# Performance work log

Hardware: AMD Instinct MI355X
Metric: run time of the kernel (lower is better)

## Reference

```python
import jax, jax.numpy as jnp
import numpy as np

N = 100000
E = 3200000
IN_C = 256
HID = 64
OUT_C = 2
EPS = 1e-5


def setup_inputs() -> dict:
    key = jax.random.key(0)
    ks = jax.random.split(key, 8)
    x = jax.random.normal(ks[0], (N, IN_C), dtype=jnp.float32)
    edge_index = jax.random.randint(ks[1], (2, E), 0, N, dtype=jnp.int64)
    # GCNConv weights (PyG: out = A_hat @ (x W) + b)
    W1 = jax.random.normal(ks[2], (IN_C, HID), dtype=jnp.float32) / np.sqrt(IN_C)
    b1 = jnp.zeros((HID,), dtype=jnp.float32)
    W2 = jax.random.normal(ks[3], (HID, OUT_C), dtype=jnp.float32) / np.sqrt(HID)
    b2 = jnp.zeros((OUT_C,), dtype=jnp.float32)
    # BatchNorm affine params
    g1 = jnp.ones((HID,), dtype=jnp.float32)
    be1 = jnp.zeros((HID,), dtype=jnp.float32)
    g2 = jnp.ones((OUT_C,), dtype=jnp.float32)
    be2 = jnp.zeros((OUT_C,), dtype=jnp.float32)
    # Decoder linear
    Wd = jax.random.normal(ks[4], (OUT_C, IN_C), dtype=jnp.float32) / np.sqrt(OUT_C)
    bd = jnp.zeros((IN_C,), dtype=jnp.float32)
    return {"x": x, "edge_index": edge_index, "W1": W1, "b1": b1, "g1": g1,
            "be1": be1, "W2": W2, "b2": b2, "g2": g2, "be2": be2,
            "Wd": Wd, "bd": bd}


def gcn_conv(x, W, b, src, dst, n):
    # x: [N, Cin] -> [N, Cout]; symmetric-normalized aggregation with self-loops
    xw = x @ W  # [N, Cout]
    loops = jnp.arange(n, dtype=src.dtype)
    s = jnp.concatenate([src, loops])  # [E+N]
    d = jnp.concatenate([dst, loops])
    deg = jax.ops.segment_sum(jnp.ones_like(d, dtype=x.dtype), d, num_segments=n)
    dinv = jax.lax.rsqrt(deg)  # deg >= 1 thanks to self-loops
    norm = dinv[s] * dinv[d]   # [E+N]
    out = jax.ops.segment_sum(norm[:, None] * xw[s], d, num_segments=n)
    return out + b


def batch_norm(x, gamma, beta):
    # training-mode BN over node dim, biased variance (torch semantics)
    mu = jnp.mean(x, axis=0)
    var = jnp.mean(jnp.square(x - mu), axis=0)
    return (x - mu) * jax.lax.rsqrt(var + EPS) * gamma + beta


def reference(x, edge_index, W1, b1, g1, be1, W2, b2, g2, be2, Wd, bd):
    src, dst = edge_index[0], edge_index[1]
    n = x.shape[0]
    h = gcn_conv(x, W1, b1, src, dst, n)
    h = jax.nn.relu(batch_norm(h, g1, be1))
    # dropout: identity (inference)
    z = batch_norm(gcn_conv(h, W2, b2, src, dst, n), g2, be2)
    return z @ Wd + bd  # decoder: [N, IN_C]
```

## Files before the change

kernel.cpp:

```cpp
#include <hip/hip_runtime.h>
#include <hip/hip_bf16.h>

#define NN 100000
#define NE 3200000
#define INC 256
#define HID 64
#define OUTC 2
#define EPSV 1e-5f

#define SCAN_CHUNK 1024
#define NBLK ((NN + SCAN_CHUNK - 1) / SCAN_CHUNK)

#define NBUCK 128
#define BCAP  26000
#define BIN_CHUNK 4096
#define BIN_K 16
#define BIN_GRID ((NE + BIN_CHUNK - 1) / BIN_CHUNK)

#define NQUART 25000

typedef short short8 __attribute__((ext_vector_type(8)));
typedef float f32x4 __attribute__((ext_vector_type(4)));

static __device__ __forceinline__ float bf2f(unsigned short u) {
    return __uint_as_float((unsigned)u << 16);
}
static __device__ __forceinline__ unsigned short f2bf(float f) {
    __hip_bfloat16 hb = __float2bfloat16(f);
    return *(unsigned short*)&hb;
}

__global__ __launch_bounds__(256) void bin_kernel(const int* __restrict__ src,
                                                  const int* __restrict__ dst,
                                                  int* __restrict__ gtail,
                                                  unsigned int* __restrict__ pbuf) {
    __shared__ int bcnt[NBUCK], bbase[NBUCK];
    int t = threadIdx.x;
    if (t < NBUCK) bcnt[t] = 0;
    __syncthreads();
    int base = blockIdx.x * BIN_CHUNK;
    int s[BIN_K], d[BIN_K], sl[BIN_K], bk[BIN_K];
#pragma unroll
    for (int r = 0; r < BIN_K; r++) {
        int i = base + r * 256 + t;
        bool v = i < NE;
        s[r] = v ? src[i] : 0;
        d[r] = v ? dst[i] : 0;
        bk[r] = (int)(((unsigned)d[r] * (unsigned)NBUCK) / (unsigned)NN);
        sl[r] = v ? atomicAdd(&bcnt[bk[r]], 1) : 0;
    }
    __syncthreads();
    if (t < NBUCK) bbase[t] = bcnt[t] ? atomicAdd(&gtail[t], bcnt[t]) : 0;
    __syncthreads();
#pragma unroll
    for (int r = 0; r < BIN_K; r++) {
        int i = base + r * 256 + t;
        if (i < NE) {
            int b = bk[r];
            int nbase = (b * NN + NBUCK - 1) >> 7;
            pbuf[(size_t)b * BCAP + bbase[b] + sl[r]] =
                ((unsigned)(d[r] - nbase) << 17) | (unsigned)s[r];
        }
    }
}

__global__ __launch_bounds__(256) void hist2_kernel(const unsigned int* __restrict__ pbuf,
                                                    const int* __restrict__ gtail,
                                                    int* __restrict__ cnt) {
    __shared__ int h[800];
    int b = blockIdx.x, t = threadIdx.x;
    int nb = (b * NN + NBUCK - 1) >> 7;
    int ne_ = ((b + 1) * NN + NBUCK - 1) >> 7;
    int range = ne_ - nb;
    for (int i = t; i < range; i += 256) h[i] = 0;
    __syncthreads();
    int ecnt = gtail[b];
    const unsigned int* p = pbuf + (size_t)b * BCAP;
    for (int i = t; i < ecnt; i += 256) atomicAdd(&h[p[i] >> 17], 1);
    __syncthreads();
    for (int i = t; i < range; i += 256) cnt[nb + i] = h[i];
}

__global__ void scan_btot_kernel(const int* __restrict__ cnt, int* __restrict__ btot) {
    __shared__ int red[4];
    int b = blockIdx.x, t = threadIdx.x;
    int base = b * SCAN_CHUNK;
    int v = 0;
    for (int j = t; j < SCAN_CHUNK; j += 256) {
        int idx = base + j;
        v += (idx < NN) ? cnt[idx] : 0;
    }
    for (int o = 32; o; o >>= 1) v += __shfl_xor(v, o);
    int wave = t >> 6, lane = t & 63;
    if (lane == 0) red[wave] = v;
    __syncthreads();
    if (t == 0) btot[b] = red[0] + red[1] + red[2] + red[3];
}

__global__ void scan_boff_kernel(const int* __restrict__ btot, int* __restrict__ boff) {
    __shared__ int wtot[2];
    int t = threadIdx.x;
    int lane = t & 63, wave = t >> 6;
    int v = (t < NBLK) ? btot[t] : 0;
    int s = v;
    for (int o = 1; o < 64; o <<= 1) {
        int u = __shfl_up(s, o);
        if (lane >= o) s += u;
    }
    if (lane == 63) wtot[wave] = s;
    __syncthreads();
    int add = (wave == 1) ? wtot[0] : 0;
    if (t < NBLK) boff[t] = s - v + add;
}

__global__ void scan_rowptr_kernel(const int* __restrict__ cnt, const int* __restrict__ boff,
                                   int* __restrict__ rowptr, float* __restrict__ dinv) {
    __shared__ int wsum[4];
    int b = blockIdx.x, t = threadIdx.x;
    int lane = t & 63, wave = t >> 6;
    int idx = b * SCAN_CHUNK + t * 4;
    int c0 = (idx + 0 < NN) ? cnt[idx + 0] : 0;
    int c1 = (idx + 1 < NN) ? cnt[idx + 1] : 0;
    int c2 = (idx + 2 < NN) ? cnt[idx + 2] : 0;
    int c3 = (idx + 3 < NN) ? cnt[idx + 3] : 0;
    int local = c0 + c1 + c2 + c3;
    int s = local;
    for (int o = 1; o < 64; o <<= 1) {
        int u = __shfl_up(s, o);
        if (lane >= o) s += u;
    }
    if (lane == 63) wsum[wave] = s;
    __syncthreads();
    if (t == 0) {
        int run = 0;
        for (int w = 0; w < 4; w++) { int x = wsum[w]; wsum[w] = run; run += x; }
    }
    __syncthreads();
    int start = boff[b] + wsum[wave] + (s - local);
    if (idx + 0 < NN) { rowptr[idx + 0] = start;                dinv[idx + 0] = rsqrtf((float)(c0 + 1)); }
    if (idx + 1 < NN) { rowptr[idx + 1] = start + c0;           dinv[idx + 1] = rsqrtf((float)(c1 + 1)); }
    if (idx + 2 < NN) { rowptr[idx + 2] = start + c0 + c1;      dinv[idx + 2] = rsqrtf((float)(c2 + 1)); }
    if (idx + 3 < NN) { rowptr[idx + 3] = start + c0 + c1 + c2; dinv[idx + 3] = rsqrtf((float)(c3 + 1)); }
    if (b == 0 && t == 0) rowptr[NN] = NE;
}

__global__ __launch_bounds__(256) void scatter2_kernel(const unsigned int* __restrict__ pbuf,
                                                       const int* __restrict__ gtail,
                                                       const int* __restrict__ rowptr,
                                                       int* __restrict__ e_src) {
    __shared__ int rp[800], fill[800];
    int b = blockIdx.x, t = threadIdx.x;
    int nb = (b * NN + NBUCK - 1) >> 7;
    int ne_ = ((b + 1) * NN + NBUCK - 1) >> 7;
    int range = ne_ - nb;
    for (int i = t; i < range; i += 256) {
        rp[i] = rowptr[nb + i];
        fill[i] = 0;
    }
    __syncthreads();
    int ecnt = gtail[b];
    const unsigned int* p = pbuf + (size_t)b * BCAP;
    for (int i = t; i < ecnt; i += 256) {
        unsigned int k = p[i];
        int loc = k >> 17;
        int pos = rp[loc] + atomicAdd(&fill[loc], 1);
        e_src[pos] = (int)(k & 0x1FFFFu);
    }
}

__global__ __launch_bounds__(256) void wprep_kernel(const float* __restrict__ W1,
                                                    unsigned short* __restrict__ Wtb) {
    int t = blockIdx.x * 256 + threadIdx.x;
    int c = t & 63;
    int k = t >> 6;
    Wtb[c * 256 + k] = f2bf(W1[k * 64 + c]);
}

#define G1_ROWS 32
#define LDP 264
__global__ __launch_bounds__(256) void gemm1_kernel(const float* __restrict__ x,
                                                    const unsigned short* __restrict__ Wtb,
                                                    const float* __restrict__ dinv,
                                                    unsigned short* __restrict__ xw1h) {
    __shared__ unsigned short xt[G1_ROWS * LDP];
    int t = threadIdx.x;
    size_t base = (size_t)blockIdx.x * G1_ROWS;

    const float4* xg = (const float4*)(x + base * INC);
#pragma unroll
    for (int ii = 0; ii < 8; ii++) {
        int idx4 = ii * 256 + t;
        float4 v = xg[idx4];
        int f = idx4 * 4;
        int row = f >> 8, k = f & 255;
        ushort4 u;
        u.x = f2bf(v.x); u.y = f2bf(v.y); u.z = f2bf(v.z); u.w = f2bf(v.w);
        *(ushort4*)(xt + row * LDP + k) = u;
    }
    __syncthreads();

    int lane = t & 63;
    int wave = t >> 6;
    int l15 = lane & 15;
    int hi = lane >> 4;
    int rgrp = wave & 1;
    int cgrp = wave >> 1;
    const unsigned short* ap = xt + (rgrp * 16 + l15) * LDP;
    const unsigned short* bp0 = Wtb + (cgrp * 32 + l15) * 256;
    const unsigned short* bp1 = bp0 + 16 * 256;
    f32x4 acc0 = {0.f, 0.f, 0.f, 0.f};
    f32x4 acc1 = {0.f, 0.f, 0.f, 0.f};
#pragma unroll
    for (int kk = 0; kk < 8; kk++) {
        int ko = kk * 32 + hi * 8;
        short8 a  = *(const short8*)(ap + ko);
        short8 b0 = *(const short8*)(bp0 + ko);
        short8 b1 = *(const short8*)(bp1 + ko);
        acc0 = __builtin_amdgcn_mfma_f32_16x16x32_bf16(a, b0, acc0, 0, 0, 0);
        acc1 = __builtin_amdgcn_mfma_f32_16x16x32_bf16(a, b1, acc1, 0, 0, 0);
    }
    unsigned short* ph = xw1h + (size_t)cgrp * NN * 32;
#pragma unroll
    for (int i = 0; i < 4; i++) {
        int grow = (int)base + rgrp * 16 + hi * 4 + i;
        float dv = dinv[grow];
        ph[(size_t)grow * 32 + l15]      = f2bf(acc0[i] * dv);
        ph[(size_t)grow * 32 + l15 + 16] = f2bf(acc1[i] * dv);
    }
}

__global__ __launch_bounds__(256) void agg1_kernel(const unsigned short* __restrict__ xw1h,
                                                   const int* __restrict__ rowptr,
                                                   const int* __restrict__ e_src,
                                                   const float* __restrict__ dinv,
                                                   const float* __restrict__ b1,
                                                   float* __restrict__ h1h,
                                                   float* __restrict__ sums1) {
    __shared__ float lsum[4][32], lsq[4][32];
    int t = threadIdx.x;
    int lane = t & 63;
    int wave = t >> 6;
    int grp = lane >> 3;
    int cl = lane & 7;
    int cohort = blockIdx.x & 7;
    int h = cohort & 1;
    int dq = cohort >> 1;
    const ushort4* plane = (const ushort4*)(xw1h + (size_t)h * NN * 32);
    float* hp = h1h + (size_t)h * NN * 32;
    float bb0 = b1[h * 32 + cl * 4 + 0];
    float bb1 = b1[h * 32 + cl * 4 + 1];
    float bb2 = b1[h * 32 + cl * 4 + 2];
    float bb3 = b1[h * 32 + cl * 4 + 3];
    int gid = ((blockIdx.x >> 3) * 4 + wave) * 8 + grp;
    int dlo = dq * NQUART;
    float ss0 = 0.f, ss1 = 0.f, ss2 = 0.f, ss3 = 0.f;
    float sq0 = 0.f, sq1 = 0.f, sq2 = 0.f, sq3 = 0.f;
    for (int d = dlo + gid; d < dlo + NQUART; d += 8192) {
        int beg = rowptr[d], end = rowptr[d + 1];
        float a0 = 0.f, a1 = 0.f, a2 = 0.f, a3 = 0.f;
        int e = beg;
        for (; e + 3 < end; e += 4) {
            int s0 = e_src[e], s1 = e_src[e + 1], s2 = e_src[e + 2], s3 = e_src[e + 3];
            ushort4 u0 = plane[(size_t)s0 * 8 + cl];
            ushort4 u1 = plane[(size_t)s1 * 8 + cl];
            ushort4 u2 = plane[(size_t)s2 * 8 + cl];
            ushort4 u3 = plane[(size_t)s3 * 8 + cl];
            a0 += bf2f(u0.x) + bf2f(u1.x) + bf2f(u2.x) + bf2f(u3.x);
            a1 += bf2f(u0.y) + bf2f(u1.y) + bf2f(u2.y) + bf2f(u3.y);
            a2 += bf2f(u0.z) + bf2f(u1.z) + bf2f(u2.z) + bf2f(u3.z);
            a3 += bf2f(u0.w) + bf2f(u1.w) + bf2f(u2.w) + bf2f(u3.w);
        }
        for (; e < end; e++) {
            int s = e_src[e];
            ushort4 u = plane[(size_t)s * 8 + cl];
            a0 += bf2f(u.x); a1 += bf2f(u.y); a2 += bf2f(u.z); a3 += bf2f(u.w);
        }
        ushort4 us = plane[(size_t)d * 8 + cl];
        a0 += bf2f(us.x); a1 += bf2f(us.y); a2 += bf2f(us.z); a3 += bf2f(us.w);
        float dv = dinv[d];
        float h0 = a0 * dv + bb0;
        float h1v = a1 * dv + bb1;
        float h2 = a2 * dv + bb2;
        float h3 = a3 * dv + bb3;
        f32x4 hv = {h0, h1v, h2, h3};
        *(f32x4*)(hp + (size_t)d * 32 + cl * 4) = hv;
        ss0 += h0; sq0 += h0 * h0;
        ss1 += h1v; sq1 += h1v * h1v;
        ss2 += h2; sq2 += h2 * h2;
        ss3 += h3; sq3 += h3 * h3;
    }
#pragma unroll
    for (int o = 8; o < 64; o <<= 1) {
        ss0 += __shfl_xor(ss0, o); sq0 += __shfl_xor(sq0, o);
        ss1 += __shfl_xor(ss1, o); sq1 += __shfl_xor(sq1, o);
        ss2 += __shfl_xor(ss2, o); sq2 += __shfl_xor(sq2, o);
        ss3 += __shfl_xor(ss3, o); sq3 += __shfl_xor(sq3, o);
    }
    if (grp == 0) {
        lsum[wave][cl * 4 + 0] = ss0; lsq[wave][cl * 4 + 0] = sq0;
        lsum[wave][cl * 4 + 1] = ss1; lsq[wave][cl * 4 + 1] = sq1;
        lsum[wave][cl * 4 + 2] = ss2; lsq[wave][cl * 4 + 2] = sq2;
        lsum[wave][cl * 4 + 3] = ss3; lsq[wave][cl * 4 + 3] = sq3;
    }
    __syncthreads();
    if (t < 32) {
        float S = lsum[0][t] + lsum[1][t] + lsum[2][t] + lsum[3][t];
        float Q = lsq[0][t] + lsq[1][t] + lsq[2][t] + lsq[3][t];
        atomicAdd(&sums1[h * 32 + t], S);
        atomicAdd(&sums1[64 + h * 32 + t], Q);
    }
}

__global__ __launch_bounds__(256) void gemm2_kernel(const float* __restrict__ h1h,
                                                    const float* __restrict__ sums1,
                                                    const float* __restrict__ g1,
                                                    const float* __restrict__ be1,
                                                    const float* __restrict__ W2,
                                                    const float* __restrict__ dinv,
                                                    float* __restrict__ xw2) {
    int lane = threadIdx.x & 63;
    int row = blockIdx.x * 4 + (threadIdx.x >> 6);
    if (row >= NN) return;
    int c = lane;
    const float invn = 1.0f / (float)NN;
    float mu = sums1[c] * invn;
    float var = sums1[64 + c] * invn - mu * mu;
    float sc = g1[c] * rsqrtf(var + EPSV);
    float sh = be1[c] - mu * sc;
    float hv = h1h[(size_t)(c >> 5) * NN * 32 + (size_t)row * 32 + (c & 31)] * sc + sh;
    hv = fmaxf(hv, 0.f);
    float p0 = hv * W2[c * 2 + 0];
    float p1 = hv * W2[c * 2 + 1];
    for (int o = 32; o; o >>= 1) {
        p0 += __shfl_xor(p0, o);
        p1 += __shfl_xor(p1, o);
    }
    if (lane == 0) {
        float dv = dinv[row];
        xw2[(size_t)row * 2 + 0] = p0 * dv;
        xw2[(size_t)row * 2 + 1] = p1 * dv;
    }
}

__global__ __launch_bounds__(256) void agg2_kernel(const float* __restrict__ xw2,
                                                   const int* __restrict__ rowptr,
                                                   const int* __restrict__ e_src,
                                                   const float* __restrict__ dinv,
                                                   const float* __restrict__ b2,
                                                   float* __restrict__ z2,
                                                   float* __restrict__ sums2) {
    __shared__ float red[4][4];
    int t = threadIdx.x;
    int lane = t & 63;
    int wave = t >> 6;
    int gl = lane & 7;
    int d = blockIdx.x * 32 + (t >> 3);
    int beg = rowptr[d], end = rowptr[d + 1];
    float a0 = 0.f, a1 = 0.f;
    int e = beg + gl;
    for (; e + 24 < end; e += 32) {
        int s0 = e_src[e], s1 = e_src[e + 8], s2 = e_src[e + 16], s3 = e_src[e + 24];
        float2 v0 = *(const float2*)(xw2 + (size_t)s0 * 2);
        float2 v1 = *(const float2*)(xw2 + (size_t)s1 * 2);
        float2 v2 = *(const float2*)(xw2 + (size_t)s2 * 2);
        float2 v3 = *(const float2*)(xw2 + (size_t)s3 * 2);
        a0 += v0.x + v1.x + v2.x + v3.x;
        a1 += v0.y + v1.y + v2.y + v3.y;
    }
    for (; e < end; e += 8) {
        int s = e_src[e];
        float2 v = *(const float2*)(xw2 + (size_t)s * 2);
        a0 += v.x;
        a1 += v.y;
    }
    if (gl == 0) {
        float2 sf = *(const float2*)(xw2 + (size_t)d * 2);
        a0 += sf.x;
        a1 += sf.y;
    }
    a0 += __shfl_xor(a0, 1); a1 += __shfl_xor(a1, 1);
    a0 += __shfl_xor(a0, 2); a1 += __shfl_xor(a1, 2);
    a0 += __shfl_xor(a0, 4); a1 += __shfl_xor(a1, 4);
    float dv = dinv[d];
    float z0 = a0 * dv + b2[0];
    float z1 = a1 * dv + b2[1];
    if (gl == 0) *(float2*)(z2 + (size_t)d * 2) = make_float2(z0, z1);
    float s0 = (gl == 0) ? z0 : 0.f;
    float s1 = (gl == 0) ? z1 : 0.f;
    float q0 = (gl == 0) ? z0 * z0 : 0.f;
    float q1 = (gl == 0) ? z1 * z1 : 0.f;
    for (int o = 8; o < 64; o <<= 1) {
        s0 += __shfl_xor(s0, o); s1 += __shfl_xor(s1, o);
        q0 += __shfl_xor(q0, o); q1 += __shfl_xor(q1, o);
    }
    if (lane == 0) { red[wave][0] = s0; red[wave][1] = s1; red[wave][2] = q0; red[wave][3] = q1; }
    __syncthreads();
    if (t < 4) {
        float v = red[0][t] + red[1][t] + red[2][t] + red[3][t];
        atomicAdd(&sums2[(blockIdx.x & 7) * 4 + t], v);
    }
}

__global__ __launch_bounds__(256) void decoder_kernel(const float* __restrict__ z2,
                                                      const float* __restrict__ sums2,
                                                      const float* __restrict__ g2,
                                                      const float* __restrict__ be2,
                                                      const float* __restrict__ Wd,
                                                      const float* __restrict__ bd,
                                                      float* __restrict__ out) {
    int g = blockIdx.x * 256 + threadIdx.x;
    int row = g >> 6;
    int c4 = (g & 63) * 4;
    float t0 = 0.f, t1 = 0.f, t2 = 0.f, t3 = 0.f;
#pragma unroll
    for (int bk = 0; bk < 8; bk++) {
        t0 += sums2[bk * 4 + 0]; t1 += sums2[bk * 4 + 1];
        t2 += sums2[bk * 4 + 2]; t3 += sums2[bk * 4 + 3];
    }
    const float invn = 1.0f / (float)NN;
    float mu0 = t0 * invn, mu1 = t1 * invn;
    float v0 = t2 * invn - mu0 * mu0;
    float v1 = t3 * invn - mu1 * mu1;
    float sc0 = g2[0] * rsqrtf(v0 + EPSV), sh0 = be2[0] - mu0 * sc0;
    float sc1 = g2[1] * rsqrtf(v1 + EPSV), sh1 = be2[1] - mu1 * sc1;
    float zb0 = z2[(size_t)row * 2 + 0] * sc0 + sh0;
    float zb1 = z2[(size_t)row * 2 + 1] * sc1 + sh1;
    float4 w0 = *(const float4*)(Wd + c4);
    float4 w1 = *(const float4*)(Wd + INC + c4);
    float4 bb = *(const float4*)(bd + c4);
    float4 o;
    o.x = zb0 * w0.x + zb1 * w1.x + bb.x;
    o.y = zb0 * w0.y + zb1 * w1.y + bb.y;
    o.z = zb0 * w0.z + zb1 * w1.z + bb.z;
    o.w = zb0 * w0.w + zb1 * w1.w + bb.w;
    *(float4*)(out + (size_t)row * INC + c4) = o;
}

static inline size_t align256(size_t x) { return (x + 255) & ~(size_t)255; }

extern "C" void kernel_launch(void* const* d_in, const int* in_sizes, int n_in,
                              void* d_out, int out_size, void* d_ws, size_t ws_size,
                              hipStream_t stream) {
    const float* x  = (const float*)d_in[0];
    const int*   ei = (const int*)d_in[1];
    const float* W1 = (const float*)d_in[2];
    const float* b1 = (const float*)d_in[3];
    const float* g1 = (const float*)d_in[4];
    const float* be1 = (const float*)d_in[5];
    const float* W2 = (const float*)d_in[6];
    const float* b2 = (const float*)d_in[7];
    const float* g2 = (const float*)d_in[8];
    const float* be2 = (const float*)d_in[9];
    const float* Wd = (const float*)d_in[10];
    const float* bd = (const float*)d_in[11];
    float* out = (float*)d_out;

    const int* src = ei;
    const int* dst = ei + NE;

    char* ws = (char*)d_ws;
    size_t off = 0;
    int* gtail = (int*)(ws + off);      off = align256(off + NBUCK * 4);
    float* sums1 = (float*)(ws + off);  off = align256(off + 128 * 4);
    float* sums2 = (float*)(ws + off);  off = align256(off + 32 * 4);
    size_t zero_bytes = off;
    int* cnt = (int*)(ws + off);        off = align256(off + NN * 4);
    int* rowptr = (int*)(ws + off);     off = align256(off + (NN + 1) * 4);
    float* dinv = (float*)(ws + off);   off = align256(off + NN * 4);
    int* btot = (int*)(ws + off);       off = align256(off + NBLK * 4);
    int* boff = (int*)(ws + off);       off = align256(off + NBLK * 4);
    unsigned short* Wtb = (unsigned short*)(ws + off); off = align256(off + (size_t)HID * INC * 2);
    unsigned int* pbuf = (unsigned int*)(ws + off); off = align256(off + (size_t)NBUCK * BCAP * 4 + 4096);
    int* e_src = (int*)(ws + off);      off = align256(off + (size_t)NE * 4 + 64);
    unsigned short* xw1h = (unsigned short*)(ws + off); off = align256(off + (size_t)NN * HID * 2);
    float* h1h = (float*)(ws + off);    off = align256(off + (size_t)NN * HID * 4);
    float* xw2 = (float*)(ws + off);    off = align256(off + (size_t)NN * 2 * 4);
    float* z2 = (float*)(ws + off);     off = align256(off + (size_t)NN * 2 * 4);
    (void)ws_size; (void)in_sizes; (void)n_in; (void)out_size;

    hipMemsetAsync(d_ws, 0, zero_bytes, stream);

    bin_kernel<<<BIN_GRID, 256, 0, stream>>>(src, dst, gtail, pbuf);
    hist2_kernel<<<NBUCK, 256, 0, stream>>>(pbuf, gtail, cnt);
    scan_btot_kernel<<<NBLK, 256, 0, stream>>>(cnt, btot);
    scan_boff_kernel<<<1, 128, 0, stream>>>(btot, boff);
    scan_rowptr_kernel<<<NBLK, 256, 0, stream>>>(cnt, boff, rowptr, dinv);
    scatter2_kernel<<<NBUCK, 256, 0, stream>>>(pbuf, gtail, rowptr, e_src);
    wprep_kernel<<<64, 256, 0, stream>>>(W1, Wtb);
    gemm1_kernel<<<NN / G1_ROWS, 256, 0, stream>>>(x, Wtb, dinv, xw1h);
    agg1_kernel<<<2048, 256, 0, stream>>>(xw1h, rowptr, e_src, dinv, b1, h1h, sums1);
    gemm2_kernel<<<(NN + 3) / 4, 256, 0, stream>>>(h1h, sums1, g1, be1, W2, dinv, xw2);
    agg2_kernel<<<NN * 8 / 256, 256, 0, stream>>>(xw2, rowptr, e_src, dinv, b2, z2, sums2);
    decoder_kernel<<<(NN * HID) / 256, 256, 0, stream>>>(z2, sums2, g2, be2, Wd, bd, out);
}
```

Baseline: 309.8 us.

## Unsplit xw1/h1 channel-halves layout and stage W1 tile in LDS for gemm1

Replaces the two 32-channel planes of xw1 and h1 with a single row-major 64-channel layout. agg1 now has 16 lanes per destination node, each gathering 128-byte full rows, and drops the cohort and quarter-range partitioning. gemm1 also stages the bf16 W1 transpose in padded shared memory instead of reading it from global memory per wave. The aim is fewer, larger random gathers per edge and cheaper B-operand loads, at the cost of losing the L2-locality the half-plane and quarter split gave.

```diff
diff --git a/kernel.cpp b/kernel.cpp
--- a/kernel.cpp
+++ b/kernel.cpp
@@ -16,8 +16,6 @@
 #define BIN_CHUNK 4096
 #define BIN_K 16
 #define BIN_GRID ((NE + BIN_CHUNK - 1) / BIN_CHUNK)
-
-#define NQUART 25000
 
 typedef short short8 __attribute__((ext_vector_type(8)));
 typedef float f32x4 __attribute__((ext_vector_type(4)));
@@ -181,8 +179,9 @@
 __global__ __launch_bounds__(256) void gemm1_kernel(const float* __restrict__ x,
                                                     const unsigned short* __restrict__ Wtb,
                                                     const float* __restrict__ dinv,
-                                                    unsigned short* __restrict__ xw1h) {
+                                                    unsigned short* __restrict__ xw1) {
     __shared__ unsigned short xt[G1_ROWS * LDP];
+    __shared__ unsigned short wt[HID * LDP];
     int t = threadIdx.x;
     size_t base = (size_t)blockIdx.x * G1_ROWS;
 
@@ -197,6 +196,15 @@
         u.x = f2bf(v.x); u.y = f2bf(v.y); u.z = f2bf(v.z); u.w = f2bf(v.w);
         *(ushort4*)(xt + row * LDP + k) = u;
     }
+    const int4* wsrc = (const int4*)Wtb;
+#pragma unroll
+    for (int ii = 0; ii < 8; ii++) {
+        int idx4 = ii * 256 + t;
+        int4 v = wsrc[idx4];
+        int e16 = idx4 * 8;
+        int c = e16 >> 8, k = e16 & 255;
+        *(int4*)(wt + c * LDP + k) = v;
+    }
     __syncthreads();
 
     int lane = t & 63;
@@ -206,8 +214,8 @@
     int rgrp = wave & 1;
     int cgrp = wave >> 1;
     const unsigned short* ap = xt + (rgrp * 16 + l15) * LDP;
-    const unsigned short* bp0 = Wtb + (cgrp * 32 + l15) * 256;
-    const unsigned short* bp1 = bp0 + 16 * 256;
+    const unsigned short* bp0 = wt + (cgrp * 32 + l15) * LDP;
+    const unsigned short* bp1 = bp0 + 16 * LDP;
     f32x4 acc0 = {0.f, 0.f, 0.f, 0.f};
     f32x4 acc1 = {0.f, 0.f, 0.f, 0.f};
 #pragma unroll
@@ -219,52 +227,47 @@
         acc0 = __builtin_amdgcn_mfma_f32_16x16x32_bf16(a, b0, acc0, 0, 0, 0);
         acc1 = __builtin_amdgcn_mfma_f32_16x16x32_bf16(a, b1, acc1, 0, 0, 0);
     }
-    unsigned short* ph = xw1h + (size_t)cgrp * NN * 32;
 #pragma unroll
     for (int i = 0; i < 4; i++) {
         int grow = (int)base + rgrp * 16 + hi * 4 + i;
         float dv = dinv[grow];
-        ph[(size_t)grow * 32 + l15]      = f2bf(acc0[i] * dv);
-        ph[(size_t)grow * 32 + l15 + 16] = f2bf(acc1[i] * dv);
-    }
-}
-
-__global__ __launch_bounds__(256) void agg1_kernel(const unsigned short* __restrict__ xw1h,
+        unsigned short* ph = xw1 + (size_t)grow * HID + cgrp * 32;
+        ph[l15]      = f2bf(acc0[i] * dv);
+        ph[l15 + 16] = f2bf(acc1[i] * dv);
+    }
+}
+
+__global__ __launch_bounds__(256) void agg1_kernel(const unsigned short* __restrict__ xw1,
                                                    const int* __restrict__ rowptr,
                                                    const int* __restrict__ e_src,
                                                    const float* __restrict__ dinv,
                                                    const float* __restrict__ b1,
-                                                   float* __restrict__ h1h,
+                                                   float* __restrict__ h1,
                                                    float* __restrict__ sums1) {
-    __shared__ float lsum[4][32], lsq[4][32];
+    __shared__ float lsum[4][64], lsq[4][64];
     int t = threadIdx.x;
     int lane = t & 63;
     int wave = t >> 6;
-    int grp = lane >> 3;
-    int cl = lane & 7;
-    int cohort = blockIdx.x & 7;
-    int h = cohort & 1;
-    int dq = cohort >> 1;
-    const ushort4* plane = (const ushort4*)(xw1h + (size_t)h * NN * 32);
-    float* hp = h1h + (size_t)h * NN * 32;
-    float bb0 = b1[h * 32 + cl * 4 + 0];
-    float bb1 = b1[h * 32 + cl * 4 + 1];
-    float bb2 = b1[h * 32 + cl * 4 + 2];
-    float bb3 = b1[h * 32 + cl * 4 + 3];
-    int gid = ((blockIdx.x >> 3) * 4 + wave) * 8 + grp;
-    int dlo = dq * NQUART;
+    int grp = lane >> 4;
+    int cl = lane & 15;
+    const ushort4* plane = (const ushort4*)xw1;
+    float bb0 = b1[cl * 4 + 0];
+    float bb1 = b1[cl * 4 + 1];
+    float bb2 = b1[cl * 4 + 2];
+    float bb3 = b1[cl * 4 + 3];
+    int gid = (blockIdx.x * 4 + wave) * 4 + grp;
     float ss0 = 0.f, ss1 = 0.f, ss2 = 0.f, ss3 = 0.f;
     float sq0 = 0.f, sq1 = 0.f, sq2 = 0.f, sq3 = 0.f;
-    for (int d = dlo + gid; d < dlo + NQUART; d += 8192) {
+    for (int d = gid; d < NN; d += 32768) {
         int beg = rowptr[d], end = rowptr[d + 1];
         float a0 = 0.f, a1 = 0.f, a2 = 0.f, a3 = 0.f;
         int e = beg;
         for (; e + 3 < end; e += 4) {
             int s0 = e_src[e], s1 = e_src[e + 1], s2 = e_src[e + 2], s3 = e_src[e + 3];
-            ushort4 u0 = plane[(size_t)s0 * 8 + cl];
-            ushort4 u1 = plane[(size_t)s1 * 8 + cl];
-            ushort4 u2 = plane[(size_t)s2 * 8 + cl];
-            ushort4 u3 = plane[(size_t)s3 * 8 + cl];
+            ushort4 u0 = plane[(size_t)s0 * 16 + cl];
+            ushort4 u1 = plane[(size_t)s1 * 16 + cl];
+            ushort4 u2 = plane[(size_t)s2 * 16 + cl];
+            ushort4 u3 = plane[(size_t)s3 * 16 + cl];
             a0 += bf2f(u0.x) + bf2f(u1.x) + bf2f(u2.x) + bf2f(u3.x);
             a1 += bf2f(u0.y) + bf2f(u1.y) + bf2f(u2.y) + bf2f(u3.y);
             a2 += bf2f(u0.z) + bf2f(u1.z) + bf2f(u2.z) + bf2f(u3.z);
@@ -272,10 +275,10 @@
         }
         for (; e < end; e++) {
             int s = e_src[e];
-            ushort4 u = plane[(size_t)s * 8 + cl];
+            ushort4 u = plane[(size_t)s * 16 + cl];
             a0 += bf2f(u.x); a1 += bf2f(u.y); a2 += bf2f(u.z); a3 += bf2f(u.w);
         }
-        ushort4 us = plane[(size_t)d * 8 + cl];
+        ushort4 us = plane[(size_t)d * 16 + cl];
         a0 += bf2f(us.x); a1 += bf2f(us.y); a2 += bf2f(us.z); a3 += bf2f(us.w);
         float dv = dinv[d];
         float h0 = a0 * dv + bb0;
@@ -283,14 +286,14 @@
         float h2 = a2 * dv + bb2;
         float h3 = a3 * dv + bb3;
         f32x4 hv = {h0, h1v, h2, h3};
-        *(f32x4*)(hp + (size_t)d * 32 + cl * 4) = hv;
+        ((f32x4*)(h1 + (size_t)d * HID))[cl] = hv;
         ss0 += h0; sq0 += h0 * h0;
         ss1 += h1v; sq1 += h1v * h1v;
         ss2 += h2; sq2 += h2 * h2;
         ss3 += h3; sq3 += h3 * h3;
     }
 #pragma unroll
-    for (int o = 8; o < 64; o <<= 1) {
+    for (int o = 16; o < 64; o <<= 1) {
         ss0 += __shfl_xor(ss0, o); sq0 += __shfl_xor(sq0, o);
         ss1 += __shfl_xor(ss1, o); sq1 += __shfl_xor(sq1, o);
         ss2 += __shfl_xor(ss2, o); sq2 += __shfl_xor(sq2, o);
@@ -303,15 +306,15 @@
         lsum[wave][cl * 4 + 3] = ss3; lsq[wave][cl * 4 + 3] = sq3;
     }
     __syncthreads();
-    if (t < 32) {
+    if (t < 64) {
         float S = lsum[0][t] + lsum[1][t] + lsum[2][t] + lsum[3][t];
         float Q = lsq[0][t] + lsq[1][t] + lsq[2][t] + lsq[3][t];
-        atomicAdd(&sums1[h * 32 + t], S);
-        atomicAdd(&sums1[64 + h * 32 + t], Q);
-    }
-}
-
-__global__ __launch_bounds__(256) void gemm2_kernel(const float* __restrict__ h1h,
+        atomicAdd(&sums1[t], S);
+        atomicAdd(&sums1[64 + t], Q);
+    }
+}
+
+__global__ __launch_bounds__(256) void gemm2_kernel(const float* __restrict__ h1,
                                                     const float* __restrict__ sums1,
                                                     const float* __restrict__ g1,
                                                     const float* __restrict__ be1,
@@ -327,7 +330,7 @@
     float var = sums1[64 + c] * invn - mu * mu;
     float sc = g1[c] * rsqrtf(var + EPSV);
     float sh = be1[c] - mu * sc;
-    float hv = h1h[(size_t)(c >> 5) * NN * 32 + (size_t)row * 32 + (c & 31)] * sc + sh;
+    float hv = h1[(size_t)row * HID + c] * sc + sh;
     hv = fmaxf(hv, 0.f);
     float p0 = hv * W2[c * 2 + 0];
     float p1 = hv * W2[c * 2 + 1];
@@ -472,8 +475,8 @@
     unsigned short* Wtb = (unsigned short*)(ws + off); off = align256(off + (size_t)HID * INC * 2);
     unsigned int* pbuf = (unsigned int*)(ws + off); off = align256(off + (size_t)NBUCK * BCAP * 4 + 4096);
     int* e_src = (int*)(ws + off);      off = align256(off + (size_t)NE * 4 + 64);
-    unsigned short* xw1h = (unsigned short*)(ws + off); off = align256(off + (size_t)NN * HID * 2);
-    float* h1h = (float*)(ws + off);    off = align256(off + (size_t)NN * HID * 4);
+    unsigned short* xw1 = (unsigned short*)(ws + off); off = align256(off + (size_t)NN * HID * 2);
+    float* h1 = (float*)(ws + off);     off = align256(off + (size_t)NN * HID * 4);
     float* xw2 = (float*)(ws + off);    off = align256(off + (size_t)NN * 2 * 4);
     float* z2 = (float*)(ws + off);     off = align256(off + (size_t)NN * 2 * 4);
     (void)ws_size; (void)in_sizes; (void)n_in; (void)out_size;
@@ -487,9 +490,9 @@
     scan_rowptr_kernel<<<NBLK, 256, 0, stream>>>(cnt, boff, rowptr, dinv);
     scatter2_kernel<<<NBUCK, 256, 0, stream>>>(pbuf, gtail, rowptr, e_src);
     wprep_kernel<<<64, 256, 0, stream>>>(W1, Wtb);
-    gemm1_kernel<<<NN / G1_ROWS, 256, 0, stream>>>(x, Wtb, dinv, xw1h);
-    agg1_kernel<<<2048, 256, 0, stream>>>(xw1h, rowptr, e_src, dinv, b1, h1h, sums1);
-    gemm2_kernel<<<(NN + 3) / 4, 256, 0, stream>>>(h1h, sums1, g1, be1, W2, dinv, xw2);
+    gemm1_kernel<<<NN / G1_ROWS, 256, 0, stream>>>(x, Wtb, dinv, xw1);
+    agg1_kernel<<<2048, 256, 0, stream>>>(xw1, rowptr, e_src, dinv, b1, h1, sums1);
+    gemm2_kernel<<<(NN + 3) / 4, 256, 0, stream>>>(h1, sums1, g1, be1, W2, dinv, xw2);
     agg2_kernel<<<NN * 8 / 256, 256, 0, stream>>>(xw2, rowptr, e_src, dinv, b2, z2, sums2);
     decoder_kernel<<<(NN * HID) / 256, 256, 0, stream>>>(z2, sums2, g2, be2, Wd, bd, out);
 }
```

Result: no change. 308.5 us (-0.4%).

## Fuse CSR histogram, scan and scatter into per-bucket build kernel; stage W1 in LDS

Applied to the files above, without the earlier changes.

Replaces the five-kernel CSR construction (histogram, three-level scan, scatter) with a tiny bucket-offset scan plus one per-bucket kernel. That kernel histograms, scans locally in shared memory, writes rowptr and dinv, and scatters sources while the bucket's packed edges are still cache-warm. This removes several launches and the global cnt round trip. Separately, gemm1 now copies the bf16 W1 tile into padded LDS instead of reading it from global memory per wave, which adds LDS use and may reduce occupancy.

```diff
diff --git a/kernel.cpp b/kernel.cpp
--- a/kernel.cpp
+++ b/kernel.cpp
@@ -7,9 +7,6 @@
 #define HID 64
 #define OUTC 2
 #define EPSV 1e-5f
-
-#define SCAN_CHUNK 1024
-#define NBLK ((NN + SCAN_CHUNK - 1) / SCAN_CHUNK)
 
 #define NBUCK 128
 #define BCAP  26000
@@ -64,10 +61,30 @@
     }
 }
 
-__global__ __launch_bounds__(256) void hist2_kernel(const unsigned int* __restrict__ pbuf,
+__global__ void bscan_kernel(const int* __restrict__ gtail, int* __restrict__ bbase) {
+    __shared__ int wtot[2];
+    int t = threadIdx.x;
+    int lane = t & 63, wave = t >> 6;
+    int v = gtail[t];
+    int s = v;
+    for (int o = 1; o < 64; o <<= 1) {
+        int u = __shfl_up(s, o);
+        if (lane >= o) s += u;
+    }
+    if (lane == 63) wtot[wave] = s;
+    __syncthreads();
+    int add = (wave == 1) ? wtot[0] : 0;
+    bbase[t] = s - v + add;
+}
+
+__global__ __launch_bounds__(256) void build_kernel(const unsigned int* __restrict__ pbuf,
                                                     const int* __restrict__ gtail,
-                                                    int* __restrict__ cnt) {
-    __shared__ int h[800];
+                                                    const int* __restrict__ bbase,
+                                                    int* __restrict__ rowptr,
+                                                    float* __restrict__ dinv,
+                                                    int* __restrict__ e_src) {
+    __shared__ int h[800], rp[800];
+    __shared__ int wsum[4];
     int b = blockIdx.x, t = threadIdx.x;
     int nb = (b * NN + NBUCK - 1) >> 7;
     int ne_ = ((b + 1) * NN + NBUCK - 1) >> 7;
@@ -78,52 +95,13 @@
     const unsigned int* p = pbuf + (size_t)b * BCAP;
     for (int i = t; i < ecnt; i += 256) atomicAdd(&h[p[i] >> 17], 1);
     __syncthreads();
-    for (int i = t; i < range; i += 256) cnt[nb + i] = h[i];
-}
-
-__global__ void scan_btot_kernel(const int* __restrict__ cnt, int* __restrict__ btot) {
-    __shared__ int red[4];
-    int b = blockIdx.x, t = threadIdx.x;
-    int base = b * SCAN_CHUNK;
-    int v = 0;
-    for (int j = t; j < SCAN_CHUNK; j += 256) {
-        int idx = base + j;
-        v += (idx < NN) ? cnt[idx] : 0;
-    }
-    for (int o = 32; o; o >>= 1) v += __shfl_xor(v, o);
-    int wave = t >> 6, lane = t & 63;
-    if (lane == 0) red[wave] = v;
-    __syncthreads();
-    if (t == 0) btot[b] = red[0] + red[1] + red[2] + red[3];
-}
-
-__global__ void scan_boff_kernel(const int* __restrict__ btot, int* __restrict__ boff) {
-    __shared__ int wtot[2];
-    int t = threadIdx.x;
+    int idx = t * 4;
+    int c0 = (idx + 0 < range) ? h[idx + 0] : 0;
+    int c1 = (idx + 1 < range) ? h[idx + 1] : 0;
+    int c2 = (idx + 2 < range) ? h[idx + 2] : 0;
+    int c3 = (idx + 3 < range) ? h[idx + 3] : 0;
+    int local = c0 + c1 + c2 + c3;
     int lane = t & 63, wave = t >> 6;
-    int v = (t < NBLK) ? btot[t] : 0;
-    int s = v;
-    for (int o = 1; o < 64; o <<= 1) {
-        int u = __shfl_up(s, o);
-        if (lane >= o) s += u;
-    }
-    if (lane == 63) wtot[wave] = s;
-    __syncthreads();
-    int add = (wave == 1) ? wtot[0] : 0;
-    if (t < NBLK) boff[t] = s - v + add;
-}
-
-__global__ void scan_rowptr_kernel(const int* __restrict__ cnt, const int* __restrict__ boff,
-                                   int* __restrict__ rowptr, float* __restrict__ dinv) {
-    __shared__ int wsum[4];
-    int b = blockIdx.x, t = threadIdx.x;
-    int lane = t & 63, wave = t >> 6;
-    int idx = b * SCAN_CHUNK + t * 4;
-    int c0 = (idx + 0 < NN) ? cnt[idx + 0] : 0;
-    int c1 = (idx + 1 < NN) ? cnt[idx + 1] : 0;
-    int c2 = (idx + 2 < NN) ? cnt[idx + 2] : 0;
-    int c3 = (idx + 3 < NN) ? cnt[idx + 3] : 0;
-    int local = c0 + c1 + c2 + c3;
     int s = local;
     for (int o = 1; o < 64; o <<= 1) {
         int u = __shfl_up(s, o);
@@ -136,34 +114,20 @@
         for (int w = 0; w < 4; w++) { int x = wsum[w]; wsum[w] = run; run += x; }
     }
     __syncthreads();
-    int start = boff[b] + wsum[wave] + (s - local);
-    if (idx + 0 < NN) { rowptr[idx + 0] = start;                dinv[idx + 0] = rsqrtf((float)(c0 + 1)); }
-    if (idx + 1 < NN) { rowptr[idx + 1] = start + c0;           dinv[idx + 1] = rsqrtf((float)(c1 + 1)); }
-    if (idx + 2 < NN) { rowptr[idx + 2] = start + c0 + c1;      dinv[idx + 2] = rsqrtf((float)(c2 + 1)); }
-    if (idx + 3 < NN) { rowptr[idx + 3] = start + c0 + c1 + c2; dinv[idx + 3] = rsqrtf((float)(c3 + 1)); }
-    if (b == 0 && t == 0) rowptr[NN] = NE;
-}
-
-__global__ __launch_bounds__(256) void scatter2_kernel(const unsigned int* __restrict__ pbuf,
-                                                       const int* __restrict__ gtail,
-                                                       const int* __restrict__ rowptr,
-                                                       int* __restrict__ e_src) {
-    __shared__ int rp[800], fill[800];
-    int b = blockIdx.x, t = threadIdx.x;
-    int nb = (b * NN + NBUCK - 1) >> 7;
-    int ne_ = ((b + 1) * NN + NBUCK - 1) >> 7;
-    int range = ne_ - nb;
-    for (int i = t; i < range; i += 256) {
-        rp[i] = rowptr[nb + i];
-        fill[i] = 0;
-    }
-    __syncthreads();
-    int ecnt = gtail[b];
-    const unsigned int* p = pbuf + (size_t)b * BCAP;
+    int start = wsum[wave] + (s - local);
+    int gb = bbase[b];
+    if (idx + 0 < range) { rp[idx + 0] = start;                rowptr[nb + idx + 0] = gb + start;                dinv[nb + idx + 0] = rsqrtf((float)(c0 + 1)); }
+    if (idx + 1 < range) { rp[idx + 1] = start + c0;           rowptr[nb + idx + 1] = gb + start + c0;           dinv[nb + idx + 1] = rsqrtf((float)(c1 + 1)); }
+    if (idx + 2 < range) { rp[idx + 2] = start + c0 + c1;      rowptr[nb + idx + 2] = gb + start + c0 + c1;      dinv[nb + idx + 2] = rsqrtf((float)(c2 + 1)); }
+    if (idx + 3 < range) { rp[idx + 3] = start + c0 + c1 + c2; rowptr[nb + idx + 3] = gb + start + c0 + c1 + c2; dinv[nb + idx + 3] = rsqrtf((float)(c3 + 1)); }
+    if (b == NBUCK - 1 && t == 0) rowptr[NN] = NE;
+    __syncthreads();
+    for (int i = t; i < range; i += 256) h[i] = 0;
+    __syncthreads();
     for (int i = t; i < ecnt; i += 256) {
         unsigned int k = p[i];
         int loc = k >> 17;
-        int pos = rp[loc] + atomicAdd(&fill[loc], 1);
+        int pos = gb + rp[loc] + atomicAdd(&h[loc], 1);
         e_src[pos] = (int)(k & 0x1FFFFu);
     }
 }
@@ -183,6 +147,7 @@
                                                     const float* __restrict__ dinv,
                                                     unsigned short* __restrict__ xw1h) {
     __shared__ unsigned short xt[G1_ROWS * LDP];
+    __shared__ unsigned short wt[HID * LDP];
     int t = threadIdx.x;
     size_t base = (size_t)blockIdx.x * G1_ROWS;
 
@@ -197,6 +162,15 @@
         u.x = f2bf(v.x); u.y = f2bf(v.y); u.z = f2bf(v.z); u.w = f2bf(v.w);
         *(ushort4*)(xt + row * LDP + k) = u;
     }
+    const int4* wsrc = (const int4*)Wtb;
+#pragma unroll
+    for (int ii = 0; ii < 8; ii++) {
+        int idx4 = ii * 256 + t;
+        int4 v = wsrc[idx4];
+        int e16 = idx4 * 8;
+        int c = e16 >> 8, k = e16 & 255;
+        *(int4*)(wt + c * LDP + k) = v;
+    }
     __syncthreads();
 
     int lane = t & 63;
@@ -206,8 +180,8 @@
     int rgrp = wave & 1;
     int cgrp = wave >> 1;
     const unsigned short* ap = xt + (rgrp * 16 + l15) * LDP;
-    const unsigned short* bp0 = Wtb + (cgrp * 32 + l15) * 256;
-    const unsigned short* bp1 = bp0 + 16 * 256;
+    const unsigned short* bp0 = wt + (cgrp * 32 + l15) * LDP;
+    const unsigned short* bp1 = bp0 + 16 * LDP;
     f32x4 acc0 = {0.f, 0.f, 0.f, 0.f};
     f32x4 acc1 = {0.f, 0.f, 0.f, 0.f};
 #pragma unroll
@@ -464,11 +438,9 @@
     float* sums1 = (float*)(ws + off);  off = align256(off + 128 * 4);
     float* sums2 = (float*)(ws + off);  off = align256(off + 32 * 4);
     size_t zero_bytes = off;
-    int* cnt = (int*)(ws + off);        off = align256(off + NN * 4);
+    int* bbase = (int*)(ws + off);      off = align256(off + NBUCK * 4);
     int* rowptr = (int*)(ws + off);     off = align256(off + (NN + 1) * 4);
     float* dinv = (float*)(ws + off);   off = align256(off + NN * 4);
-    int* btot = (int*)(ws + off);       off = align256(off + NBLK * 4);
-    int* boff = (int*)(ws + off);       off = align256(off + NBLK * 4);
     unsigned short* Wtb = (unsigned short*)(ws + off); off = align256(off + (size_t)HID * INC * 2);
     unsigned int* pbuf = (unsigned int*)(ws + off); off = align256(off + (size_t)NBUCK * BCAP * 4 + 4096);
     int* e_src = (int*)(ws + off);      off = align256(off + (size_t)NE * 4 + 64);
@@ -481,11 +453,8 @@
     hipMemsetAsync(d_ws, 0, zero_bytes, stream);
 
     bin_kernel<<<BIN_GRID, 256, 0, stream>>>(src, dst, gtail, pbuf);
-    hist2_kernel<<<NBUCK, 256, 0, stream>>>(pbuf, gtail, cnt);
-    scan_btot_kernel<<<NBLK, 256, 0, stream>>>(cnt, btot);
-    scan_boff_kernel<<<1, 128, 0, stream>>>(btot, boff);
-    scan_rowptr_kernel<<<NBLK, 256, 0, stream>>>(cnt, boff, rowptr, dinv);
-    scatter2_kernel<<<NBUCK, 256, 0, stream>>>(pbuf, gtail, rowptr, e_src);
+    bscan_kernel<<<1, 128, 0, stream>>>(gtail, bbase);
+    build_kernel<<<NBUCK, 256, 0, stream>>>(pbuf, gtail, bbase, rowptr, dinv, e_src);
     wprep_kernel<<<64, 256, 0, stream>>>(W1, Wtb);
     gemm1_kernel<<<NN / G1_ROWS, 256, 0, stream>>>(x, Wtb, dinv, xw1h);
     agg1_kernel<<<2048, 256, 0, stream>>>(xw1h, rowptr, e_src, dinv, b1, h1h, sums1);
```

Result: faster. 292.5 us (-5.6%).
